# Kernel tuning notes

Measured on AMD Instinct MI355X. Metric: run time of the kernel, lower is better.

Reference implementation:

```python
import jax, jax.numpy as jnp
import numpy as np

D_MODEL = 256
D_STATE = 64
R_MIN, R_MAX, MAX_PHASE = 0.0, 1.0, 6.28


def setup_inputs() -> dict:
    key = jax.random.key(0)
    ks = jax.random.split(key, 8)
    u1 = jax.random.uniform(ks[0], (D_STATE,), dtype=jnp.float32)
    u2 = jax.random.uniform(ks[1], (D_STATE,), dtype=jnp.float32)
    nu_log = jnp.log(-0.5 * jnp.log(u1 * (R_MAX**2 - R_MIN**2) + R_MIN**2))
    theta_log = jnp.log(u2 * MAX_PHASE)
    sB = 1.0 / np.sqrt(2 * D_STATE)
    sC = 1.0 / np.sqrt(D_STATE)
    B_re = jax.random.normal(ks[2], (D_MODEL, D_STATE), dtype=jnp.float32) * sB
    B_im = jax.random.normal(ks[3], (D_MODEL, D_STATE), dtype=jnp.float32) * sB
    C_re = jax.random.normal(ks[4], (D_MODEL, D_STATE), dtype=jnp.float32) * sC
    C_im = jax.random.normal(ks[5], (D_MODEL, D_STATE), dtype=jnp.float32) * sC
    D = jax.random.normal(ks[6], (D_MODEL,), dtype=jnp.float32)
    x = jax.random.normal(ks[7], (4, 8192, D_MODEL), dtype=jnp.float32)
    return {"x": x, "nu_log": nu_log, "theta_log": theta_log,
            "B_re": B_re, "B_im": B_im, "C_re": C_re, "C_im": C_im, "D": D}


def reference(x, nu_log, theta_log, B_re, B_im, C_re, C_im, D):
    B, L, H = x.shape
    # diagonal transition: Lambda = exp(-exp(nu) + i*exp(theta)); Lambda^k = exp(k*log_lambda)
    log_lambda = -jnp.exp(nu_log) + 1j * jnp.exp(theta_log)          # (n,)
    k = jnp.arange(L, dtype=jnp.float32)
    Lambda_k = jnp.exp(k[:, None] * log_lambda[None, :])              # (L, n) complex
    CB = (C_re + 1j * C_im) * (B_re + 1j * B_im)                      # (H, n)
    kernels = jnp.einsum('hn,ln->hl', CB, Lambda_k).real              # (H, L)
    # FFT (causal, linear) convolution per channel
    n_fft = 2 * L
    x_f = jnp.fft.rfft(x, n=n_fft, axis=1)                            # (B, L+1, H)
    k_f = jnp.fft.rfft(kernels, n=n_fft, axis=1)                      # (H, L+1)
    y_f = x_f * k_f.T[None]                                           # (B, L+1, H)
    y = jnp.fft.irfft(y_f, n=n_fft, axis=1)[:, :L, :]
    return y + x * D[None, None, :]
```

## Files before the change

kernel.cpp:

```cpp
#include <hip/hip_runtime.h>
#include <hip/hip_bf16.h>

#define BB   4
#define LL   8192
#define HH   256
#define NN   64
#define NSEG 128
#define LSEG 64

typedef __attribute__((ext_vector_type(8))) short  short8;
typedef __attribute__((ext_vector_type(4))) float  float4v;
typedef __attribute__((ext_vector_type(4))) int    int4v;


__device__ __forceinline__ float ldF(const void* p, size_t i, int isbf) {
    return isbf ? __bfloat162float(((const __hip_bfloat16*)p)[i])
                : ((const float*)p)[i];
}

__global__ void k_sniff(const void* p0, const void* p1, const void* p2,
                        const void* p3, const void* p4, const void* p5,
                        const void* p6, const void* p7, int* flags)
{
    int t = threadIdx.x;
    if (t < 8) {
        const void* ps[8] = {p0, p1, p2, p3, p4, p5, p6, p7};
        const unsigned int* d = (const unsigned int*)ps[t];
        int nbf = 0, nrand = 0;
        for (int i = 0; i < 32; ++i) {
            unsigned int lo = d[i] & 0xFFFFu;
            unsigned int e  = (lo >> 7) & 0xFFu;
            if (lo == 0u) {  }
            else if (e >= 90u && e <= 140u) nbf++;
            else nrand++;
        }
        flags[t] = (nrand == 0 && nbf >= 8) ? 1 : 0;
    }
}

__global__ __launch_bounds__(256) void k_setup(
    const void* nu_log, const void* theta_log,
    const void* B_re, const void* B_im,
    const void* C_re, const void* C_im,
    const void* D, const int* __restrict__ flags,
    float* lam, float* lam64, float* Df, float* CBt,
    float* PsegRe, float* PsegIm)
{
    int t = blockIdx.x * 256 + threadIdx.x;
    if (t < NN) {
        float nu = expf(ldF(nu_log, t, flags[1]));
        float th = expf(ldF(theta_log, t, flags[2]));
        float a  = expf(-nu);
        lam[2*t]   = a * cosf(th);
        lam[2*t+1] = a * sinf(th);
        float a64 = expf(-64.0f * nu);
        float ph  = 64.0f * th;
        lam64[2*t]   = a64 * cosf(ph);
        lam64[2*t+1] = a64 * sinf(ph);
    }
    if (t < HH) Df[t] = ldF(D, t, flags[7]);
    if (t < HH * NN) {
        int h = t >> 6, n = t & 63;
        float bre = ldF(B_re, h*NN+n, flags[3]);
        float bim = ldF(B_im, h*NN+n, flags[4]);
        float cre = ldF(C_re, h*NN+n, flags[5]);
        float cim = ldF(C_im, h*NN+n, flags[6]);
        CBt[(n*2+0)*HH + h] = cre*bre - cim*bim;
        CBt[(n*2+1)*HH + h] = cre*bim + cim*bre;
    }
    if (t < 64 * 64) {
        int l = t >> 6, n = t & 63;
        float nu = expf(ldF(nu_log, n, flags[1]));
        float th = expf(ldF(theta_log, n, flags[2]));
        float fp = (float)(63 - l);
        float ar = expf(-fp * nu);
        PsegRe[t] = ar * cosf(fp * th);
        PsegIm[t] = ar * sinf(fp * th);
    }
}

__global__ __launch_bounds__(256) void k_ktab(
    const float* __restrict__ CBt, const float* __restrict__ PsegRe,
    const float* __restrict__ PsegIm, const float* __restrict__ lam64,
    float* __restrict__ Ktab,
    short* __restrict__ VreT, short* __restrict__ VimnT,
    short* __restrict__ PreH, short* __restrict__ PreL,
    short* __restrict__ PimH, short* __restrict__ PimL)
{
    int t = blockIdx.x * 256 + threadIdx.x;
    int h = t >> 6, j = t & 63;
    float acc = 0.f;
    for (int n = 0; n < NN; ++n)
        acc += CBt[(2*n)*HH + h]   * PsegRe[(63-j)*64 + n]
             - CBt[(2*n+1)*HH + h] * PsegIm[(63-j)*64 + n];
    Ktab[j*HH + h] = acc;
    if (t < 64*64) {
        int tau = t >> 6, n = t & 63;
        float vr, vi;
        if (tau < 63) {
            vr =  PsegRe[(62-tau)*64 + n];
            vi = -PsegIm[(62-tau)*64 + n];
        } else {
            vr =  lam64[2*n];
            vi = -lam64[2*n+1];
        }
        __hip_bfloat16 br = __float2bfloat16(vr);
        __hip_bfloat16 bi = __float2bfloat16(vi);
        VreT[tau*64 + n]  = *(short*)&br;
        VimnT[tau*64 + n] = *(short*)&bi;

        int n2 = t >> 6, l2 = t & 63;
        float pr = PsegRe[l2*64 + n2];
        float pi = PsegIm[l2*64 + n2];
        __hip_bfloat16 prh = __float2bfloat16(pr);
        __hip_bfloat16 prl = __float2bfloat16(pr - __bfloat162float(prh));
        __hip_bfloat16 pih = __float2bfloat16(pi);
        __hip_bfloat16 pil = __float2bfloat16(pi - __bfloat162float(pih));
        PreH[t] = *(short*)&prh;
        PreL[t] = *(short*)&prl;
        PimH[t] = *(short*)&pih;
        PimL[t] = *(short*)&pil;
    }
}

template<bool ISBF>
__device__ __forceinline__ void segsum_body(
    const void* __restrict__ x, size_t xbase,
    const short* __restrict__ PreH, const short* __restrict__ PreL,
    const short* __restrict__ PimH, const short* __restrict__ PimL,
    __hip_bfloat16* __restrict__ Abuf, size_t abase, int q, int l15)
{
    #pragma unroll
    for (int nt = 0; nt < 4; ++nt) {
        short8 xh[2], xl[2];
        #pragma unroll
        for (int ks = 0; ks < 2; ++ks)
            #pragma unroll
            for (int j = 0; j < 8; ++j) {
                size_t a = xbase + nt*16 + (size_t)(ks*32 + q*8 + j)*HH;
                if (ISBF) {
                    xh[ks][j] = ((const short*)x)[a];
                } else {
                    float xf = ((const float*)x)[a];
                    __hip_bfloat16 hv = __float2bfloat16(xf);
                    __hip_bfloat16 lv = __float2bfloat16(xf - __bfloat162float(hv));
                    xh[ks][j] = *(short*)&hv;
                    xl[ks][j] = *(short*)&lv;
                }
            }
        #pragma unroll
        for (int mt = 0; mt < 4; ++mt) {
            float4v ar = {0.f, 0.f, 0.f, 0.f};
            float4v ai = {0.f, 0.f, 0.f, 0.f};
            #pragma unroll
            for (int ks = 0; ks < 2; ++ks) {
                int off = (mt*16 + l15)*64 + ks*32 + q*8;
                short8 prh = *(const short8*)(PreH + off);
                short8 pih = *(const short8*)(PimH + off);
                short8 prl = *(const short8*)(PreL + off);
                short8 pil = *(const short8*)(PimL + off);
                ar = __builtin_amdgcn_mfma_f32_16x16x32_bf16(prh, xh[ks], ar, 0, 0, 0);
                ai = __builtin_amdgcn_mfma_f32_16x16x32_bf16(pih, xh[ks], ai, 0, 0, 0);
                ar = __builtin_amdgcn_mfma_f32_16x16x32_bf16(prl, xh[ks], ar, 0, 0, 0);
                ai = __builtin_amdgcn_mfma_f32_16x16x32_bf16(pil, xh[ks], ai, 0, 0, 0);
                if (!ISBF) {
                    ar = __builtin_amdgcn_mfma_f32_16x16x32_bf16(prh, xl[ks], ar, 0, 0, 0);
                    ai = __builtin_amdgcn_mfma_f32_16x16x32_bf16(pih, xl[ks], ai, 0, 0, 0);
                }
            }
            #pragma unroll
            for (int r = 0; r < 4; ++r) {
                int n = mt*16 + q*4 + r;
                Abuf[abase + (size_t)n*128 + nt*16 + l15]      = __float2bfloat16(ar[r]);
                Abuf[abase + (size_t)n*128 + 64 + nt*16 + l15] = __float2bfloat16(ai[r]);
            }
        }
    }
}

__global__ __launch_bounds__(256) void k_segsum(
    const void* __restrict__ x,
    const short* __restrict__ PreH, const short* __restrict__ PreL,
    const short* __restrict__ PimH, const short* __restrict__ PimL,
    const int* __restrict__ flags, __hip_bfloat16* __restrict__ Abuf)
{
    int bk = blockIdx.x;
    int s  = bk & (NSEG - 1);
    int b  = bk >> 7;
    int w    = threadIdx.x >> 6;
    int lane = threadIdx.x & 63;
    int q = lane >> 4, l15 = lane & 15;

    size_t xbase = ((size_t)(b*LL) + s*64) * HH + w*64 + l15;
    size_t abase = (((size_t)(b*4 + w) * NSEG + s) * NN) * 128;

    if (flags[0]) segsum_body<true >(x, xbase, PreH, PreL, PimH, PimL, Abuf, abase, q, l15);
    else          segsum_body<false>(x, xbase, PreH, PreL, PimH, PimL, Abuf, abase, q, l15);
}

__global__ __launch_bounds__(256) void k_scan(
    const float* __restrict__ lam64, const float* __restrict__ CBt,
    __hip_bfloat16* __restrict__ Abuf)
{
    int w    = blockIdx.x * 4 + (threadIdx.x >> 6);
    int lane = threadIdx.x & 63;
    int n    = w & 63;
    int hg   = (w >> 6) & 3;
    int b    = w >> 8;
    int h    = hg*64 + lane;

    float lre = lam64[2*n], lim = lam64[2*n+1];
    float cbre = CBt[(2*n)*HH + h], cbim = CBt[(2*n+1)*HH + h];
    float sre = 0.f, sim = 0.f;
    size_t base0 = (((size_t)(b*4 + hg) * NSEG) * NN + n) * 128 + lane;
    for (int s = 0; s < NSEG; ++s) {
        size_t base = base0 + (size_t)s * NN * 128;
        float are = __bfloat162float(Abuf[base]);
        float aim = __bfloat162float(Abuf[base + 64]);
        float ure = cbre*sre - cbim*sim;
        float uim = cbre*sim + cbim*sre;
        Abuf[base]      = __float2bfloat16(ure);
        Abuf[base + 64] = __float2bfloat16(uim);
        float t = fmaf(lre, sre, fmaf(-lim, sim, are));
        sim = fmaf(lre, sim, fmaf(lim, sre, aim));
        sre = t;
    }
}

__global__ __launch_bounds__(256) void k_carry(
    const short* __restrict__ VreT, const short* __restrict__ VimnT,
    const short* __restrict__ U, float* __restrict__ y)
{
    int bk = blockIdx.x;
    int s  = bk & (NSEG - 1);
    int b  = bk >> 7;
    int w    = threadIdx.x >> 6;
    int lane = threadIdx.x & 63;
    int q = lane >> 4, l15 = lane & 15;
    size_t ubase = (((size_t)(b*4 + w) * NSEG + s) * NN) * 128;

    short8 afr[4][2], afi[4][2];
    #pragma unroll
    for (int mt = 0; mt < 4; ++mt)
        #pragma unroll
        for (int ks = 0; ks < 2; ++ks) {
            int off = (mt*16 + l15)*64 + ks*32 + q*8;
            afr[mt][ks] = *(const short8*)(VreT + off);
            afi[mt][ks] = *(const short8*)(VimnT + off);
        }

    #pragma unroll
    for (int nt = 0; nt < 4; ++nt) {
        int l = nt*16 + l15;
        short8 bre[2], bim[2];
        #pragma unroll
        for (int ks = 0; ks < 2; ++ks)
            #pragma unroll
            for (int j = 0; j < 8; ++j) {
                int n = ks*32 + q*8 + j;
                bre[ks][j] = U[ubase + (size_t)n*128 + l];
                bim[ks][j] = U[ubase + (size_t)n*128 + 64 + l];
            }
        int h = w*64 + l;
        #pragma unroll
        for (int mt = 0; mt < 4; ++mt) {
            float4v acc = {0.f, 0.f, 0.f, 0.f};
            #pragma unroll
            for (int ks = 0; ks < 2; ++ks) {
                acc = __builtin_amdgcn_mfma_f32_16x16x32_bf16(afr[mt][ks], bre[ks], acc, 0, 0, 0);
                acc = __builtin_amdgcn_mfma_f32_16x16x32_bf16(afi[mt][ks], bim[ks], acc, 0, 0, 0);
            }
            #pragma unroll
            for (int r = 0; r < 4; ++r) {
                int tau = mt*16 + q*4 + r;
                y[((size_t)b*LL + s*64 + tau)*HH + h] = acc[r];
            }
        }
    }
}

template<bool ISBF, int U>
__device__ __forceinline__ void conv_u(
    const void* __restrict__ x, const float* __restrict__ Df,
    const float* __restrict__ Ktab, const short* __restrict__ xs,
    int b, int s, int h, float* __restrict__ y)
{
    int g0 = s*64 + U*16;
    size_t rbase = ((size_t)b*LL + g0)*HH + h;
    float xv[16], yv[16];
    float dh = Df[h];
    #pragma unroll
    for (int t = 0; t < 16; ++t) {
        float xl;
        if (ISBF) xl = __bfloat162float(((const __hip_bfloat16*)x)[rbase + (size_t)t*HH]);
        else      xl = ((const float*)x)[rbase + (size_t)t*HH];
        xv[t] = xl;
        yv[t] = fmaf(dh, xl, y[rbase + (size_t)t*HH]);
    }
    float kreg[16*U + 16];
    #pragma unroll
    for (int j = 0; j < 16*U + 16; ++j) kreg[j] = Ktab[j*HH + h];
    #pragma unroll
    for (int j = 0; j < 16; ++j)
        #pragma unroll
        for (int t = j; t < 16; ++t) yv[t] = fmaf(kreg[j], xv[t-j], yv[t]);
    #pragma unroll
    for (int m = 0; m < 16*U; ++m) {
        short bits = xs[(U*16 - 1 - m)*HH + h];
        float xm = __bfloat162float(*(const __hip_bfloat16*)&bits);
        #pragma unroll
        for (int t = 0; t < 16; ++t) yv[t] = fmaf(kreg[t+1+m], xm, yv[t]);
    }
    #pragma unroll
    for (int t = 0; t < 16; ++t) y[rbase + (size_t)t*HH] = yv[t];
}

template<bool ISBF>
__device__ __forceinline__ void conv_block(
    const void* __restrict__ x, const float* __restrict__ Df,
    const float* __restrict__ Ktab, short* xs, int b, int s,
    float* __restrict__ y)
{
    int t = threadIdx.x;
    size_t sb = ((size_t)b*LL + s*64) * HH;
    if (ISBF) {
        const int4v* xp = (const int4v*)((const __hip_bfloat16*)x + sb);
        int4v* xd = (int4v*)xs;
        xd[t]        = xp[t];
        xd[t + 1024] = xp[t + 1024];
    } else {
        const float* xp = (const float*)x + sb;
        #pragma unroll
        for (int i = 0; i < 2; ++i) {
            int e = (t + i*1024) * 8;
            #pragma unroll
            for (int j = 0; j < 8; ++j) {
                __hip_bfloat16 v = __float2bfloat16(xp[e + j]);
                xs[e + j] = *(short*)&v;
            }
        }
    }
    __syncthreads();
    int w = t >> 6, lane = t & 63;
    int u = w >> 2, hg = w & 3;
    int h = hg*64 + lane;
    switch (u) {
        case 0: conv_u<ISBF,0>(x, Df, Ktab, xs, b, s, h, y); break;
        case 1: conv_u<ISBF,1>(x, Df, Ktab, xs, b, s, h, y); break;
        case 2: conv_u<ISBF,2>(x, Df, Ktab, xs, b, s, h, y); break;
        case 3: conv_u<ISBF,3>(x, Df, Ktab, xs, b, s, h, y); break;
    }
}

__global__ __launch_bounds__(1024) void k_conv(
    const void* __restrict__ x, const float* __restrict__ Df,
    const float* __restrict__ Ktab, const int* __restrict__ flags,
    float* __restrict__ y)
{
    __shared__ short xs[64 * HH];
    int bk = blockIdx.x;
    int s  = bk & (NSEG - 1);
    int b  = bk >> 7;
    if (flags[0]) conv_block<true >(x, Df, Ktab, xs, b, s, y);
    else          conv_block<false>(x, Df, Ktab, xs, b, s, y);
}

extern "C" void kernel_launch(void* const* d_in, const int* in_sizes, int n_in,
                              void* d_out, int out_size, void* d_ws, size_t ws_size,
                              hipStream_t stream)
{
    const void* x  = d_in[0];
    const void* nu = d_in[1];
    const void* th = d_in[2];
    const void* Br = d_in[3];
    const void* Bi = d_in[4];
    const void* Cr = d_in[5];
    const void* Ci = d_in[6];
    const void* D  = d_in[7];

    char* ws = (char*)d_ws;
    float* lam    = (float*)(ws);
    float* lam64  = (float*)(ws + 512);
    int*   flags  = (int*)(ws + 1024);
    float* Df     = (float*)(ws + 1088);
    float* CBt    = (float*)(ws + 2112);
    float* Ktab   = (float*)(ws + 133184);
    short* VreT   = (short*)(ws + 198720);
    short* VimnT  = (short*)(ws + 206912);
    float* PsegRe = (float*)(ws + 215104);
    float* PsegIm = (float*)(ws + 231744);
    short* PreH   = (short*)(ws + 248128);
    short* PreL   = (short*)(ws + 256320);
    short* PimH   = (short*)(ws + 264512);
    short* PimL   = (short*)(ws + 272704);
    __hip_bfloat16* Abuf = (__hip_bfloat16*)(ws + 294912);
    float* yout = (float*)d_out;

    k_sniff<<<dim3(1), dim3(64), 0, stream>>>(x, nu, th, Br, Bi, Cr, Ci, D, flags);
    k_setup<<<dim3(64), dim3(256), 0, stream>>>(nu, th, Br, Bi, Cr, Ci, D, flags,
                                                lam, lam64, Df, CBt, PsegRe, PsegIm);
    k_ktab<<<dim3(64), dim3(256), 0, stream>>>(CBt, PsegRe, PsegIm, lam64,
                                               Ktab, VreT, VimnT,
                                               PreH, PreL, PimH, PimL);
    k_segsum<<<dim3(512), dim3(256), 0, stream>>>(x, PreH, PreL, PimH, PimL,
                                                  flags, Abuf);
    k_scan<<<dim3(256), dim3(256), 0, stream>>>(lam64, CBt, Abuf);
    k_carry<<<dim3(512), dim3(256), 0, stream>>>(VreT, VimnT, (const short*)Abuf, yout);
    k_conv<<<dim3(512), dim3(1024), 0, stream>>>(x, Df, Ktab, flags, yout);
}
```

Baseline: 202.0 us.

## Fuse carry MFMA into conv kernel via shared memory and prefetch scan loads

Merges the carry kernel (MFMA projection of scanned states) into the intra-segment convolution kernel, so each block writes the carry contribution into a 64KB shared buffer instead of round-tripping it through global y. The scan kernel also software-prefetches the next 16 segment states into registers, which hides load latency in its serial recurrence. In exchange, shared memory per block grows to 96KB, which may limit occupancy, and the scan uses more registers.

```diff
diff --git a/kernel.cpp b/kernel.cpp
--- a/kernel.cpp
+++ b/kernel.cpp
@@ -213,69 +213,38 @@
     float cbre = CBt[(2*n)*HH + h], cbim = CBt[(2*n+1)*HH + h];
     float sre = 0.f, sim = 0.f;
     size_t base0 = (((size_t)(b*4 + hg) * NSEG) * NN + n) * 128 + lane;
-    for (int s = 0; s < NSEG; ++s) {
-        size_t base = base0 + (size_t)s * NN * 128;
-        float are = __bfloat162float(Abuf[base]);
-        float aim = __bfloat162float(Abuf[base + 64]);
-        float ure = cbre*sre - cbim*sim;
-        float uim = cbre*sim + cbim*sre;
-        Abuf[base]      = __float2bfloat16(ure);
-        Abuf[base + 64] = __float2bfloat16(uim);
-        float t = fmaf(lre, sre, fmaf(-lim, sim, are));
-        sim = fmaf(lre, sim, fmaf(lim, sre, aim));
-        sre = t;
-    }
-}
-
-__global__ __launch_bounds__(256) void k_carry(
-    const short* __restrict__ VreT, const short* __restrict__ VimnT,
-    const short* __restrict__ U, float* __restrict__ y)
-{
-    int bk = blockIdx.x;
-    int s  = bk & (NSEG - 1);
-    int b  = bk >> 7;
-    int w    = threadIdx.x >> 6;
-    int lane = threadIdx.x & 63;
-    int q = lane >> 4, l15 = lane & 15;
-    size_t ubase = (((size_t)(b*4 + w) * NSEG + s) * NN) * 128;
-
-    short8 afr[4][2], afi[4][2];
-    #pragma unroll
-    for (int mt = 0; mt < 4; ++mt)
-        #pragma unroll
-        for (int ks = 0; ks < 2; ++ks) {
-            int off = (mt*16 + l15)*64 + ks*32 + q*8;
-            afr[mt][ks] = *(const short8*)(VreT + off);
-            afi[mt][ks] = *(const short8*)(VimnT + off);
-        }
-
-    #pragma unroll
-    for (int nt = 0; nt < 4; ++nt) {
-        int l = nt*16 + l15;
-        short8 bre[2], bim[2];
-        #pragma unroll
-        for (int ks = 0; ks < 2; ++ks)
+
+    float curR[16], curI[16], nxtR[16], nxtI[16];
+    #pragma unroll
+    for (int k = 0; k < 16; ++k) {
+        size_t base = base0 + (size_t)k * NN * 128;
+        curR[k] = __bfloat162float(Abuf[base]);
+        curI[k] = __bfloat162float(Abuf[base + 64]);
+    }
+    #pragma unroll
+    for (int blk = 0; blk < 8; ++blk) {
+        if (blk < 7) {
             #pragma unroll
-            for (int j = 0; j < 8; ++j) {
-                int n = ks*32 + q*8 + j;
-                bre[ks][j] = U[ubase + (size_t)n*128 + l];
-                bim[ks][j] = U[ubase + (size_t)n*128 + 64 + l];
+            for (int k = 0; k < 16; ++k) {
+                size_t base = base0 + (size_t)((blk+1)*16 + k) * NN * 128;
+                nxtR[k] = __bfloat162float(Abuf[base]);
+                nxtI[k] = __bfloat162float(Abuf[base + 64]);
             }
-        int h = w*64 + l;
-        #pragma unroll
-        for (int mt = 0; mt < 4; ++mt) {
-            float4v acc = {0.f, 0.f, 0.f, 0.f};
-            #pragma unroll
-            for (int ks = 0; ks < 2; ++ks) {
-                acc = __builtin_amdgcn_mfma_f32_16x16x32_bf16(afr[mt][ks], bre[ks], acc, 0, 0, 0);
-                acc = __builtin_amdgcn_mfma_f32_16x16x32_bf16(afi[mt][ks], bim[ks], acc, 0, 0, 0);
-            }
-            #pragma unroll
-            for (int r = 0; r < 4; ++r) {
-                int tau = mt*16 + q*4 + r;
-                y[((size_t)b*LL + s*64 + tau)*HH + h] = acc[r];
-            }
-        }
+        }
+        #pragma unroll
+        for (int k = 0; k < 16; ++k) {
+            size_t base = base0 + (size_t)(blk*16 + k) * NN * 128;
+            float are = curR[k], aim = curI[k];
+            float ure = cbre*sre - cbim*sim;
+            float uim = cbre*sim + cbim*sre;
+            Abuf[base]      = __float2bfloat16(ure);
+            Abuf[base + 64] = __float2bfloat16(uim);
+            float t2 = fmaf(lre, sre, fmaf(-lim, sim, are));
+            sim = fmaf(lre, sim, fmaf(lim, sre, aim));
+            sre = t2;
+        }
+        #pragma unroll
+        for (int k = 0; k < 16; ++k) { curR[k] = nxtR[k]; curI[k] = nxtI[k]; }
     }
 }
 
@@ -283,6 +252,7 @@
 __device__ __forceinline__ void conv_u(
     const void* __restrict__ x, const float* __restrict__ Df,
     const float* __restrict__ Ktab, const short* __restrict__ xs,
+    const float* __restrict__ yc,
     int b, int s, int h, float* __restrict__ y)
 {
     int g0 = s*64 + U*16;
@@ -295,7 +265,7 @@
         if (ISBF) xl = __bfloat162float(((const __hip_bfloat16*)x)[rbase + (size_t)t*HH]);
         else      xl = ((const float*)x)[rbase + (size_t)t*HH];
         xv[t] = xl;
-        yv[t] = fmaf(dh, xl, y[rbase + (size_t)t*HH]);
+        yv[t] = fmaf(dh, xl, yc[(U*16 + t)*HH + h]);
     }
     float kreg[16*U + 16];
     #pragma unroll
@@ -316,12 +286,14 @@
 }
 
 template<bool ISBF>
-__device__ __forceinline__ void conv_block(
-    const void* __restrict__ x, const float* __restrict__ Df,
-    const float* __restrict__ Ktab, short* xs, int b, int s,
-    float* __restrict__ y)
+__device__ __forceinline__ void cc_body(
+    const short* __restrict__ VreT, const short* __restrict__ VimnT,
+    const short* __restrict__ Ubuf, const void* __restrict__ x,
+    const float* __restrict__ Df, const float* __restrict__ Ktab,
+    float* yc, short* xs, int b, int s, float* __restrict__ y)
 {
     int t = threadIdx.x;
+
     size_t sb = ((size_t)b*LL + s*64) * HH;
     if (ISBF) {
         const int4v* xp = (const int4v*)((const __hip_bfloat16*)x + sb);
@@ -340,29 +312,66 @@
             }
         }
     }
+
+    int w = t >> 6, lane = t & 63;
+    int hg = w & 3, nt = w >> 2;
+    int q = lane >> 4, l15 = lane & 15;
+    size_t ubase = (((size_t)(b*4 + hg) * NSEG + s) * NN) * 128;
+
+    int l = nt*16 + l15;
+    short8 bre[2], bim[2];
+    #pragma unroll
+    for (int ks = 0; ks < 2; ++ks)
+        #pragma unroll
+        for (int j = 0; j < 8; ++j) {
+            int n = ks*32 + q*8 + j;
+            bre[ks][j] = Ubuf[ubase + (size_t)n*128 + l];
+            bim[ks][j] = Ubuf[ubase + (size_t)n*128 + 64 + l];
+        }
+    int h = hg*64 + l;
+    #pragma unroll
+    for (int mt = 0; mt < 4; ++mt) {
+        float4v acc = {0.f, 0.f, 0.f, 0.f};
+        #pragma unroll
+        for (int ks = 0; ks < 2; ++ks) {
+            int off = (mt*16 + l15)*64 + ks*32 + q*8;
+            short8 afr = *(const short8*)(VreT + off);
+            short8 afi = *(const short8*)(VimnT + off);
+            acc = __builtin_amdgcn_mfma_f32_16x16x32_bf16(afr, bre[ks], acc, 0, 0, 0);
+            acc = __builtin_amdgcn_mfma_f32_16x16x32_bf16(afi, bim[ks], acc, 0, 0, 0);
+        }
+        #pragma unroll
+        for (int r = 0; r < 4; ++r) {
+            int tau = mt*16 + q*4 + r;
+            yc[tau*HH + h] = acc[r];
+        }
+    }
+
     __syncthreads();
-    int w = t >> 6, lane = t & 63;
-    int u = w >> 2, hg = w & 3;
-    int h = hg*64 + lane;
+
+    int u = w >> 2;
+    int h2 = hg*64 + lane;
     switch (u) {
-        case 0: conv_u<ISBF,0>(x, Df, Ktab, xs, b, s, h, y); break;
-        case 1: conv_u<ISBF,1>(x, Df, Ktab, xs, b, s, h, y); break;
-        case 2: conv_u<ISBF,2>(x, Df, Ktab, xs, b, s, h, y); break;
-        case 3: conv_u<ISBF,3>(x, Df, Ktab, xs, b, s, h, y); break;
-    }
-}
-
-__global__ __launch_bounds__(1024) void k_conv(
-    const void* __restrict__ x, const float* __restrict__ Df,
-    const float* __restrict__ Ktab, const int* __restrict__ flags,
-    float* __restrict__ y)
-{
+        case 0: conv_u<ISBF,0>(x, Df, Ktab, xs, yc, b, s, h2, y); break;
+        case 1: conv_u<ISBF,1>(x, Df, Ktab, xs, yc, b, s, h2, y); break;
+        case 2: conv_u<ISBF,2>(x, Df, Ktab, xs, yc, b, s, h2, y); break;
+        case 3: conv_u<ISBF,3>(x, Df, Ktab, xs, yc, b, s, h2, y); break;
+    }
+}
+
+__global__ __launch_bounds__(1024) void k_cc(
+    const short* __restrict__ VreT, const short* __restrict__ VimnT,
+    const short* __restrict__ Ubuf, const void* __restrict__ x,
+    const float* __restrict__ Df, const float* __restrict__ Ktab,
+    const int* __restrict__ flags, float* __restrict__ y)
+{
+    __shared__ float yc[64 * HH];
     __shared__ short xs[64 * HH];
     int bk = blockIdx.x;
     int s  = bk & (NSEG - 1);
     int b  = bk >> 7;
-    if (flags[0]) conv_block<true >(x, Df, Ktab, xs, b, s, y);
-    else          conv_block<false>(x, Df, Ktab, xs, b, s, y);
+    if (flags[0]) cc_body<true >(VreT, VimnT, Ubuf, x, Df, Ktab, yc, xs, b, s, y);
+    else          cc_body<false>(VreT, VimnT, Ubuf, x, Df, Ktab, yc, xs, b, s, y);
 }
 
 extern "C" void kernel_launch(void* const* d_in, const int* in_sizes, int n_in,
@@ -405,6 +414,6 @@
     k_segsum<<<dim3(512), dim3(256), 0, stream>>>(x, PreH, PreL, PimH, PimL,
                                                   flags, Abuf);
     k_scan<<<dim3(256), dim3(256), 0, stream>>>(lam64, CBt, Abuf);
-    k_carry<<<dim3(512), dim3(256), 0, stream>>>(VreT, VimnT, (const short*)Abuf, yout);
-    k_conv<<<dim3(512), dim3(1024), 0, stream>>>(x, Df, Ktab, flags, yout);
-}
+    k_cc<<<dim3(512), dim3(1024), 0, stream>>>(VreT, VimnT, (const short*)Abuf,
+                                               x, Df, Ktab, flags, yout);
+}
```

Result: faster. 188.7 us (-6.6%).
